# Kernel optimization log

Hardware: AMD Instinct MI355X
Metric: run time of the kernel (lower is better)

## Reference

```python
import jax, jax.numpy as jnp
import numpy as np

N, E, G = 50000, 800000, 512
HD, ED, GD, HID = 128, 64, 64, 128  # h_dim, e_dim, g_dim, hid_dim


def _mlp2(x, W1, b1, W2, b2, last_act):
    # Linear -> ReLU -> Linear (-> optional last activation)
    y = jax.nn.relu(x @ W1 + b1) @ W2 + b2
    return last_act(y) if last_act is not None else y


def setup_inputs() -> dict:
    key = jax.random.key(0)
    ks = list(jax.random.split(key, 24))
    ki = iter(ks)

    def p(shape):
        return (jax.random.normal(next(ki), shape, jnp.float32) * 0.02)

    inp = {
        "h": jax.random.normal(next(ki), (N, HD), jnp.float32),
        "e_index": jax.random.randint(next(ki), (2, E), 0, N),
        "e": jax.random.normal(next(ki), (E, ED), jnp.float32),
        "g": jax.random.normal(next(ki), (G, GD), jnp.float32),
        "batch": jnp.sort(jax.random.randint(next(ki), (N,), 0, G)),
        # fc_m: [2*HD+ED+GD, HID, HID], last_activation=relu
        "W_m1": p((2 * HD + ED + GD, HID)), "b_m1": jnp.zeros((HID,), jnp.float32),
        "W_m2": p((HID, HID)), "b_m2": jnp.zeros((HID,), jnp.float32),
        # fc_m_att: [HID, 1], sigmoid
        "W_ma": p((HID, 1)), "b_ma": jnp.zeros((1,), jnp.float32),
        # fc_e: [HID, ED, ED]
        "W_e1": p((HID, ED)), "b_e1": jnp.zeros((ED,), jnp.float32),
        "W_e2": p((ED, ED)), "b_e2": jnp.zeros((ED,), jnp.float32),
        # fc_h: [HD+HID+GD, HD, HD]
        "W_h1": p((HD + HID + GD, HD)), "b_h1": jnp.zeros((HD,), jnp.float32),
        "W_h2": p((HD, HD)), "b_h2": jnp.zeros((HD,), jnp.float32),
        # fc_h_att: [HD, 1]
        "W_ha": p((HD, 1)), "b_ha": jnp.zeros((1,), jnp.float32),
        # fc_g: [GD+HD, GD, GD]
        "W_g1": p((GD + HD, GD)), "b_g1": jnp.zeros((GD,), jnp.float32),
        "W_g2": p((GD, GD)), "b_g2": jnp.zeros((GD,), jnp.float32),
    }
    return inp


def reference(h, e_index, e, g, batch,
              W_m1, b_m1, W_m2, b_m2, W_ma, b_ma,
              W_e1, b_e1, W_e2, b_e2,
              W_h1, b_h1, W_h2, b_h2, W_ha, b_ha,
              W_g1, b_g1, W_g2, b_g2):
    src, dst = e_index[0], e_index[1]
    e_batch = batch[dst]

    # edge message: concat gathered endpoints + edge feat + gathered global
    m_cat = jnp.concatenate([h[src], h[dst], e, g[e_batch]], axis=1)  # [E, 2HD+ED+GD]
    m = jax.nn.relu(jax.nn.relu(m_cat @ W_m1 + b_m1) @ W_m2 + b_m2)   # [E, HID]
    m_att = jax.nn.sigmoid(m @ W_ma + b_ma)                            # [E, 1]

    e_update = _mlp2(m, W_e1, b_e1, W_e2, b_e2, None)                  # [E, ED]
    e_out = jax.nn.relu(e + e_update)

    m_aggr = jax.ops.segment_sum(m_att * m, dst, num_segments=h.shape[0])  # [N, HID]

    h_cat = jnp.concatenate([h, m_aggr, g[batch]], axis=1)             # [N, HD+HID+GD]
    h_update = _mlp2(h_cat, W_h1, b_h1, W_h2, b_h2, None)
    h_out = jax.nn.relu(h + h_update)                                  # [N, HD]
    h_att = h_out @ W_ha + b_ha                                        # [N, 1]

    h_aggr = jax.ops.segment_sum(h_att * h_out, batch, num_segments=g.shape[0])  # [G, HD]

    g_cat = jnp.concatenate([g, h_aggr], axis=1)                       # [G, GD+HD]
    g_update = _mlp2(g_cat, W_g1, b_g1, W_g2, b_g2, None)
    g_out = jax.nn.relu(g + g_update)

    return (h_out, e_out, g_out)
```

## Files before the change

### kernel.cpp

```cpp
#include <hip/hip_runtime.h>
#include <hip/hip_bf16.h>

#define NN 50000
#define NE 800000
#define NG 512
#define HD 128
#define ED 64
#define GD 64
#define HID 128

typedef __attribute__((ext_vector_type(8))) short short8;
typedef __attribute__((ext_vector_type(4))) float f32x4;

__device__ __forceinline__ short f2bf(float f) {
  union { float f; unsigned u; } v; v.f = f;
  unsigned r = v.u + 0x7fffu + ((v.u >> 16) & 1u);
  return (short)(r >> 16);
}

__device__ __forceinline__ short8 load_a8(const float* p) {
  const f32x4* q = (const f32x4*)p;
  f32x4 x0 = q[0], x1 = q[1];
  short8 r;
  r[0]=f2bf(x0[0]); r[1]=f2bf(x0[1]); r[2]=f2bf(x0[2]); r[3]=f2bf(x0[3]);
  r[4]=f2bf(x1[0]); r[5]=f2bf(x1[1]); r[6]=f2bf(x1[2]); r[7]=f2bf(x1[3]);
  return r;
}

__device__ __forceinline__ int swz(int row, int col, int rowBytes) {
  int b = row * rowBytes + col * 2;
  b ^= (row & 7) << 4;
  return b >> 1;
}

__global__ void pack_kernel(const float* __restrict__ Wm1, const float* __restrict__ Wm2,
                            const float* __restrict__ We1, const float* __restrict__ We2,
                            const float* __restrict__ Wh1, const float* __restrict__ Wh2,
                            short* __restrict__ out) {
  int gid = blockIdx.x * 256 + threadIdx.x;
  if (gid >= 135168) return;
  const float* W; int Ncol, base, idx;
  if (gid < 49152)       { W = Wm1; Ncol = 128; base = 0;      idx = gid; }
  else if (gid < 65536)  { W = Wm2; Ncol = 128; base = 49152;  idx = gid - 49152; }
  else if (gid < 73728)  { W = We1; Ncol = 64;  base = 65536;  idx = gid - 65536; }
  else if (gid < 77824)  { W = We2; Ncol = 64;  base = 73728;  idx = gid - 73728; }
  else if (gid < 118784) { W = Wh1; Ncol = 128; base = 77824;  idx = gid - 77824; }
  else                   { W = Wh2; Ncol = 128; base = 118784; idx = gid - 118784; }
  int k = idx / Ncol, n = idx % Ncol;
  out[base + (k >> 3) * Ncol * 8 + n * 8 + (k & 7)] = f2bf(W[idx]);
}

__global__ __launch_bounds__(256) void edge_kernel(
    const float* __restrict__ h, const int* __restrict__ ei,
    const float* __restrict__ e, const float* __restrict__ g,
    const int* __restrict__ batch,
    const short* __restrict__ pWm1, const float* __restrict__ bm1,
    const short* __restrict__ pWm2, const float* __restrict__ bm2,
    const float* __restrict__ Wma, const float* __restrict__ bma,
    const short* __restrict__ pWe1, const float* __restrict__ be1,
    const short* __restrict__ pWe2, const float* __restrict__ be2,
    float* __restrict__ e_out, float* __restrict__ m_aggr) {
  __shared__ short lds_m[4][16 * 128];
  __shared__ short lds_t[4][16 * 64];

  const int wave = threadIdx.x >> 6;
  const int lane = threadIdx.x & 63;
  const int row16 = lane & 15;
  const int quad = lane >> 4;
  const int ebase = blockIdx.x * 64 + wave * 16;

  const int eidA = ebase + row16;
  const int srcA = ei[eidA];
  const int dstA = ei[NE + eidA];
  const int gbA = batch[dstA];

  const float* seg0 = h + (size_t)srcA * HD;
  const float* seg1 = h + (size_t)dstA * HD;
  const float* seg2 = e + (size_t)eidA * ED;
  const float* seg3 = g + (size_t)gbA * GD;

  f32x4 acc[8];
#pragma unroll
  for (int t = 0; t < 8; ++t) acc[t] = (f32x4)0.0f;
#pragma unroll
  for (int c = 0; c < 12; ++c) {
    const float* src; int off;
    if (c < 4)       { src = seg0; off = c * 32; }
    else if (c < 8)  { src = seg1; off = (c - 4) * 32; }
    else if (c < 10) { src = seg2; off = (c - 8) * 32; }
    else             { src = seg3; off = (c - 10) * 32; }
    short8 a = load_a8(src + off + quad * 8);
    const short* bp = pWm1 + (size_t)(c * 4 + quad) * HID * 8 + row16 * 8;
#pragma unroll
    for (int t = 0; t < 8; ++t) {
      short8 b = *(const short8*)(bp + t * 16 * 8);
      acc[t] = __builtin_amdgcn_mfma_f32_16x16x32_bf16(a, b, acc[t], 0, 0, 0);
    }
  }
#pragma unroll
  for (int t = 0; t < 8; ++t) {
    float b1 = bm1[t * 16 + row16];
#pragma unroll
    for (int r = 0; r < 4; ++r) {
      float y = fmaxf(acc[t][r] + b1, 0.f);
      lds_m[wave][swz(quad * 4 + r, t * 16 + row16, 256)] = f2bf(y);
    }
  }
  __syncthreads();

  f32x4 acc2[8];
#pragma unroll
  for (int t = 0; t < 8; ++t) acc2[t] = (f32x4)0.0f;
#pragma unroll
  for (int c = 0; c < 4; ++c) {
    short8 a = *(const short8*)&lds_m[wave][swz(row16, c * 32 + quad * 8, 256)];
    const short* bp = pWm2 + 49152 * 0 + (size_t)(c * 4 + quad) * HID * 8 + row16 * 8;
#pragma unroll
    for (int t = 0; t < 8; ++t) {
      short8 b = *(const short8*)(bp + t * 16 * 8);
      acc2[t] = __builtin_amdgcn_mfma_f32_16x16x32_bf16(a, b, acc2[t], 0, 0, 0);
    }
  }
  __syncthreads();
  float mval[8][4];
#pragma unroll
  for (int t = 0; t < 8; ++t) {
    float b2 = bm2[t * 16 + row16];
#pragma unroll
    for (int r = 0; r < 4; ++r) {
      float y = fmaxf(acc2[t][r] + b2, 0.f);
      mval[t][r] = y;
      lds_m[wave][swz(quad * 4 + r, t * 16 + row16, 256)] = f2bf(y);
    }
  }
  __syncthreads();

  float part[4] = {0.f, 0.f, 0.f, 0.f};
#pragma unroll
  for (int t = 0; t < 8; ++t) {
    float w = Wma[t * 16 + row16];
#pragma unroll
    for (int r = 0; r < 4; ++r) part[r] += mval[t][r] * w;
  }
#pragma unroll
  for (int s = 1; s < 16; s <<= 1) {
#pragma unroll
    for (int r = 0; r < 4; ++r) part[r] += __shfl_xor(part[r], s, 64);
  }
  float bma0 = bma[0];
  float attv[4];
#pragma unroll
  for (int r = 0; r < 4; ++r) attv[r] = 1.f / (1.f + __expf(-(part[r] + bma0)));

  int dstS[4];
#pragma unroll
  for (int r = 0; r < 4; ++r) dstS[r] = ei[NE + ebase + quad * 4 + r];
#pragma unroll
  for (int t = 0; t < 8; ++t)
#pragma unroll
    for (int r = 0; r < 4; ++r)
      atomicAdd(&m_aggr[(size_t)dstS[r] * HID + t * 16 + row16], attv[r] * mval[t][r]);

  f32x4 acc3[4];
#pragma unroll
  for (int t = 0; t < 4; ++t) acc3[t] = (f32x4)0.0f;
#pragma unroll
  for (int c = 0; c < 4; ++c) {
    short8 a = *(const short8*)&lds_m[wave][swz(row16, c * 32 + quad * 8, 256)];
    const short* bp = pWe1 + (size_t)(c * 4 + quad) * ED * 8 + row16 * 8;
#pragma unroll
    for (int t = 0; t < 4; ++t) {
      short8 b = *(const short8*)(bp + t * 16 * 8);
      acc3[t] = __builtin_amdgcn_mfma_f32_16x16x32_bf16(a, b, acc3[t], 0, 0, 0);
    }
  }
#pragma unroll
  for (int t = 0; t < 4; ++t) {
    float b1 = be1[t * 16 + row16];
#pragma unroll
    for (int r = 0; r < 4; ++r) {
      float y = fmaxf(acc3[t][r] + b1, 0.f);
      lds_t[wave][swz(quad * 4 + r, t * 16 + row16, 128)] = f2bf(y);
    }
  }
  __syncthreads();

  f32x4 acc4[4];
#pragma unroll
  for (int t = 0; t < 4; ++t) acc4[t] = (f32x4)0.0f;
#pragma unroll
  for (int c = 0; c < 2; ++c) {
    short8 a = *(const short8*)&lds_t[wave][swz(row16, c * 32 + quad * 8, 128)];
    const short* bp = pWe2 + (size_t)(c * 4 + quad) * ED * 8 + row16 * 8;
#pragma unroll
    for (int t = 0; t < 4; ++t) {
      short8 b = *(const short8*)(bp + t * 16 * 8);
      acc4[t] = __builtin_amdgcn_mfma_f32_16x16x32_bf16(a, b, acc4[t], 0, 0, 0);
    }
  }
#pragma unroll
  for (int t = 0; t < 4; ++t) {
    float b2 = be2[t * 16 + row16];
#pragma unroll
    for (int r = 0; r < 4; ++r) {
      int erow = ebase + quad * 4 + r;
      int col = t * 16 + row16;
      float v = e[(size_t)erow * ED + col] + acc4[t][r] + b2;
      e_out[(size_t)erow * ED + col] = fmaxf(v, 0.f);
    }
  }
}

__global__ __launch_bounds__(256) void node_kernel(
    const float* __restrict__ h, const float* __restrict__ m_aggr,
    const float* __restrict__ g, const int* __restrict__ batch,
    const short* __restrict__ pWh1, const float* __restrict__ bh1,
    const short* __restrict__ pWh2, const float* __restrict__ bh2,
    const float* __restrict__ Wha, const float* __restrict__ bha,
    float* __restrict__ h_out, float* __restrict__ h_aggr) {
  __shared__ short lds_y[4][16 * 128];

  const int wave = threadIdx.x >> 6;
  const int lane = threadIdx.x & 63;
  const int row16 = lane & 15;
  const int quad = lane >> 4;
  const int nbase = blockIdx.x * 64 + wave * 16;

  int nA = nbase + row16;
  int nAc = nA < NN ? nA : NN - 1;
  int gbA = batch[nAc];
  const float* seg0 = h + (size_t)nAc * HD;
  const float* seg1 = m_aggr + (size_t)nAc * HID;
  const float* seg2 = g + (size_t)gbA * GD;

  f32x4 acc[8];
#pragma unroll
  for (int t = 0; t < 8; ++t) acc[t] = (f32x4)0.0f;
#pragma unroll
  for (int c = 0; c < 10; ++c) {
    const float* src; int off;
    if (c < 4)      { src = seg0; off = c * 32; }
    else if (c < 8) { src = seg1; off = (c - 4) * 32; }
    else            { src = seg2; off = (c - 8) * 32; }
    short8 a = load_a8(src + off + quad * 8);
    const short* bp = pWh1 + (size_t)(c * 4 + quad) * HD * 8 + row16 * 8;
#pragma unroll
    for (int t = 0; t < 8; ++t) {
      short8 b = *(const short8*)(bp + t * 16 * 8);
      acc[t] = __builtin_amdgcn_mfma_f32_16x16x32_bf16(a, b, acc[t], 0, 0, 0);
    }
  }
#pragma unroll
  for (int t = 0; t < 8; ++t) {
    float b1 = bh1[t * 16 + row16];
#pragma unroll
    for (int r = 0; r < 4; ++r) {
      float y = fmaxf(acc[t][r] + b1, 0.f);
      lds_y[wave][swz(quad * 4 + r, t * 16 + row16, 256)] = f2bf(y);
    }
  }
  __syncthreads();

  f32x4 acc2[8];
#pragma unroll
  for (int t = 0; t < 8; ++t) acc2[t] = (f32x4)0.0f;
#pragma unroll
  for (int c = 0; c < 4; ++c) {
    short8 a = *(const short8*)&lds_y[wave][swz(row16, c * 32 + quad * 8, 256)];
    const short* bp = pWh2 + (size_t)(c * 4 + quad) * HD * 8 + row16 * 8;
#pragma unroll
    for (int t = 0; t < 8; ++t) {
      short8 b = *(const short8*)(bp + t * 16 * 8);
      acc2[t] = __builtin_amdgcn_mfma_f32_16x16x32_bf16(a, b, acc2[t], 0, 0, 0);
    }
  }

  float hval[8][4];
  int nS[4];
#pragma unroll
  for (int r = 0; r < 4; ++r) nS[r] = nbase + quad * 4 + r;
#pragma unroll
  for (int t = 0; t < 8; ++t) {
    float b2 = bh2[t * 16 + row16];
#pragma unroll
    for (int r = 0; r < 4; ++r) {
      float v = 0.f;
      if (nS[r] < NN) {
        v = h[(size_t)nS[r] * HD + t * 16 + row16] + acc2[t][r] + b2;
        v = fmaxf(v, 0.f);
        h_out[(size_t)nS[r] * HD + t * 16 + row16] = v;
      }
      hval[t][r] = v;
    }
  }

  float part[4] = {0.f, 0.f, 0.f, 0.f};
#pragma unroll
  for (int t = 0; t < 8; ++t) {
    float w = Wha[t * 16 + row16];
#pragma unroll
    for (int r = 0; r < 4; ++r) part[r] += hval[t][r] * w;
  }
#pragma unroll
  for (int s = 1; s < 16; s <<= 1) {
#pragma unroll
    for (int r = 0; r < 4; ++r) part[r] += __shfl_xor(part[r], s, 64);
  }
  float bha0 = bha[0];
  int bS[4];
#pragma unroll
  for (int r = 0; r < 4; ++r) bS[r] = (nS[r] < NN) ? batch[nS[r]] : 0;
#pragma unroll
  for (int t = 0; t < 8; ++t)
#pragma unroll
    for (int r = 0; r < 4; ++r)
      if (nS[r] < NN)
        atomicAdd(&h_aggr[(size_t)bS[r] * HD + t * 16 + row16],
                  (part[r] + bha0) * hval[t][r]);
}

__global__ void g_kernel(const float* __restrict__ g, const float* __restrict__ h_aggr,
                         const float* __restrict__ Wg1, const float* __restrict__ bg1,
                         const float* __restrict__ Wg2, const float* __restrict__ bg2,
                         float* __restrict__ g_out) {
  __shared__ float cat[192];
  __shared__ float y1[64];
  int r = blockIdx.x;
  int t = threadIdx.x;
  cat[t] = g[(size_t)r * GD + t];
  cat[64 + t] = h_aggr[(size_t)r * HD + t];
  cat[128 + t] = h_aggr[(size_t)r * HD + 64 + t];
  __syncthreads();
  float a = bg1[t];
  for (int k = 0; k < 192; ++k) a += cat[k] * Wg1[k * 64 + t];
  y1[t] = fmaxf(a, 0.f);
  __syncthreads();
  float b = bg2[t];
  for (int k = 0; k < 64; ++k) b += y1[k] * Wg2[k * 64 + t];
  float v = g[(size_t)r * GD + t] + b;
  g_out[(size_t)r * GD + t] = fmaxf(v, 0.f);
}

extern "C" void kernel_launch(void* const* d_in, const int* in_sizes, int n_in,
                              void* d_out, int out_size, void* d_ws, size_t ws_size,
                              hipStream_t stream) {
  const float* h = (const float*)d_in[0];
  const int* ei = (const int*)d_in[1];
  const float* e = (const float*)d_in[2];
  const float* g = (const float*)d_in[3];
  const int* batch = (const int*)d_in[4];
  const float* Wm1 = (const float*)d_in[5];
  const float* bm1 = (const float*)d_in[6];
  const float* Wm2 = (const float*)d_in[7];
  const float* bm2 = (const float*)d_in[8];
  const float* Wma = (const float*)d_in[9];
  const float* bma = (const float*)d_in[10];
  const float* We1 = (const float*)d_in[11];
  const float* be1 = (const float*)d_in[12];
  const float* We2 = (const float*)d_in[13];
  const float* be2 = (const float*)d_in[14];
  const float* Wh1 = (const float*)d_in[15];
  const float* bh1 = (const float*)d_in[16];
  const float* Wh2 = (const float*)d_in[17];
  const float* bh2 = (const float*)d_in[18];
  const float* Wha = (const float*)d_in[19];
  const float* bha = (const float*)d_in[20];
  const float* Wg1 = (const float*)d_in[21];
  const float* bg1 = (const float*)d_in[22];
  const float* Wg2 = (const float*)d_in[23];
  const float* bg2 = (const float*)d_in[24];

  float* out = (float*)d_out;
  float* h_out = out;
  float* e_out = out + (size_t)NN * HD;
  float* g_out = e_out + (size_t)NE * ED;

  char* ws = (char*)d_ws;
  float* m_aggr = (float*)ws;
  float* h_aggr = (float*)(ws + 25600000);
  short* packed = (short*)(ws + 25862144);
  short* pWm1 = packed;
  short* pWm2 = packed + 49152;
  short* pWe1 = packed + 65536;
  short* pWe2 = packed + 73728;
  short* pWh1 = packed + 77824;
  short* pWh2 = packed + 118784;

  hipMemsetAsync(m_aggr, 0, (size_t)NN * HID * 4, stream);
  hipMemsetAsync(h_aggr, 0, (size_t)NG * HD * 4, stream);

  pack_kernel<<<(135168 + 255) / 256, 256, 0, stream>>>(Wm1, Wm2, We1, We2, Wh1, Wh2, packed);

  edge_kernel<<<NE / 64, 256, 0, stream>>>(h, ei, e, g, batch,
                                           pWm1, bm1, pWm2, bm2, Wma, bma,
                                           pWe1, be1, pWe2, be2, e_out, m_aggr);

  node_kernel<<<(NN + 63) / 64, 256, 0, stream>>>(h, m_aggr, g, batch,
                                                  pWh1, bh1, pWh2, bh2, Wha, bha,
                                                  h_out, h_aggr);

  g_kernel<<<NG, 64, 0, stream>>>(g, h_aggr, Wg1, bg1, Wg2, bg2, g_out);
}
```

Baseline: 755.0 us.

## Sort edges by destination and replace per-element atomics with block segmented reduction

Adds a counting sort of edges by destination node (count, single-block scan, scatter) so that each edge block processes edges grouped by dst. Attention-weighted messages are staged in LDS as bf16 and reduced per destination segment by 128 threads. Only boundary segments use atomics; segments fully inside the block are written with plain stores. The same segmented reduction replaces the per-element atomics into h_aggr in the node kernel, and several block barriers around wave-private LDS are dropped. In exchange it adds preprocessing kernels, scattered e/e_out row access through the permutation, and bf16 rounding of the aggregated contributions.

```diff
diff --git a/kernel.cpp b/kernel.cpp
--- a/kernel.cpp
+++ b/kernel.cpp
@@ -16,6 +16,12 @@
   union { float f; unsigned u; } v; v.f = f;
   unsigned r = v.u + 0x7fffu + ((v.u >> 16) & 1u);
   return (short)(r >> 16);
+}
+
+__device__ __forceinline__ float bf2f(short s) {
+  union { unsigned u; float f; } v;
+  v.u = ((unsigned)(unsigned short)s) << 16;
+  return v.f;
 }
 
 __device__ __forceinline__ short8 load_a8(const float* p) {
@@ -50,10 +56,44 @@
   out[base + (k >> 3) * Ncol * 8 + n * 8 + (k & 7)] = f2bf(W[idx]);
 }
 
+__global__ void count_kernel(const int* __restrict__ ei, int* __restrict__ deg) {
+  int i = blockIdx.x * 256 + threadIdx.x;
+  if (i < NE) atomicAdd(&deg[ei[NE + i]], 1);
+}
+
+__global__ __launch_bounds__(1024) void scan_kernel(int* __restrict__ deg) {
+  __shared__ int psum[1024];
+  const int CH = 49;
+  int t = threadIdx.x;
+  int lo = t * CH, hi = lo + CH; if (hi > NN) hi = NN; if (lo > NN) lo = NN;
+  int s = 0;
+  for (int i = lo; i < hi; ++i) s += deg[i];
+  psum[t] = s;
+  __syncthreads();
+  for (int d = 1; d < 1024; d <<= 1) {
+    int v = (t >= d) ? psum[t - d] : 0;
+    __syncthreads();
+    psum[t] += v;
+    __syncthreads();
+  }
+  int run = (t == 0) ? 0 : psum[t - 1];
+  for (int i = lo; i < hi; ++i) { int v = deg[i]; deg[i] = run; run += v; }
+}
+
+__global__ void scatter_kernel(const int* __restrict__ ei, int* __restrict__ off,
+                               int* __restrict__ elist) {
+  int i = blockIdx.x * 256 + threadIdx.x;
+  if (i < NE) {
+    int d = ei[NE + i];
+    int p = atomicAdd(&off[d], 1);
+    elist[p] = i;
+  }
+}
+
 __global__ __launch_bounds__(256) void edge_kernel(
     const float* __restrict__ h, const int* __restrict__ ei,
     const float* __restrict__ e, const float* __restrict__ g,
-    const int* __restrict__ batch,
+    const int* __restrict__ batch, const int* __restrict__ elist,
     const short* __restrict__ pWm1, const float* __restrict__ bm1,
     const short* __restrict__ pWm2, const float* __restrict__ bm2,
     const float* __restrict__ Wma, const float* __restrict__ bma,
@@ -62,17 +102,20 @@
     float* __restrict__ e_out, float* __restrict__ m_aggr) {
   __shared__ short lds_m[4][16 * 128];
   __shared__ short lds_t[4][16 * 64];
+  __shared__ short lds_w[64 * 132];
+  __shared__ int sdst[64];
 
   const int wave = threadIdx.x >> 6;
   const int lane = threadIdx.x & 63;
   const int row16 = lane & 15;
   const int quad = lane >> 4;
-  const int ebase = blockIdx.x * 64 + wave * 16;
-
-  const int eidA = ebase + row16;
+  const int pbase = blockIdx.x * 64 + wave * 16;
+
+  const int eidA = elist[pbase + row16];
   const int srcA = ei[eidA];
   const int dstA = ei[NE + eidA];
   const int gbA = batch[dstA];
+  if (quad == 0) sdst[wave * 16 + row16] = dstA;
 
   const float* seg0 = h + (size_t)srcA * HD;
   const float* seg1 = h + (size_t)dstA * HD;
@@ -106,7 +149,6 @@
       lds_m[wave][swz(quad * 4 + r, t * 16 + row16, 256)] = f2bf(y);
     }
   }
-  __syncthreads();
 
   f32x4 acc2[8];
 #pragma unroll
@@ -114,14 +156,14 @@
 #pragma unroll
   for (int c = 0; c < 4; ++c) {
     short8 a = *(const short8*)&lds_m[wave][swz(row16, c * 32 + quad * 8, 256)];
-    const short* bp = pWm2 + 49152 * 0 + (size_t)(c * 4 + quad) * HID * 8 + row16 * 8;
+    const short* bp = pWm2 + (size_t)(c * 4 + quad) * HID * 8 + row16 * 8;
 #pragma unroll
     for (int t = 0; t < 8; ++t) {
       short8 b = *(const short8*)(bp + t * 16 * 8);
       acc2[t] = __builtin_amdgcn_mfma_f32_16x16x32_bf16(a, b, acc2[t], 0, 0, 0);
     }
   }
-  __syncthreads();
+
   float mval[8][4];
 #pragma unroll
   for (int t = 0; t < 8; ++t) {
@@ -133,7 +175,6 @@
       lds_m[wave][swz(quad * 4 + r, t * 16 + row16, 256)] = f2bf(y);
     }
   }
-  __syncthreads();
 
   float part[4] = {0.f, 0.f, 0.f, 0.f};
 #pragma unroll
@@ -152,14 +193,33 @@
 #pragma unroll
   for (int r = 0; r < 4; ++r) attv[r] = 1.f / (1.f + __expf(-(part[r] + bma0)));
 
-  int dstS[4];
-#pragma unroll
-  for (int r = 0; r < 4; ++r) dstS[r] = ei[NE + ebase + quad * 4 + r];
 #pragma unroll
   for (int t = 0; t < 8; ++t)
 #pragma unroll
     for (int r = 0; r < 4; ++r)
-      atomicAdd(&m_aggr[(size_t)dstS[r] * HID + t * 16 + row16], attv[r] * mval[t][r]);
+      lds_w[(wave * 16 + quad * 4 + r) * 132 + t * 16 + row16] = f2bf(attv[r] * mval[t][r]);
+
+  __syncthreads();
+
+  if (threadIdx.x < 128) {
+    int col = threadIdx.x;
+    int cur = sdst[0];
+    float sum = 0.f;
+    int segs = 0;
+#pragma unroll 1
+    for (int r = 0; r < 64; ++r) {
+      int d = sdst[r];
+      float v = bf2f(lds_w[r * 132 + col]);
+      if (d != cur) {
+        if (segs == 0) atomicAdd(&m_aggr[(size_t)cur * HID + col], sum);
+        else m_aggr[(size_t)cur * HID + col] = sum;
+        cur = d; sum = v; segs = r;
+      } else {
+        sum += v;
+      }
+    }
+    atomicAdd(&m_aggr[(size_t)cur * HID + col], sum);
+  }
 
   f32x4 acc3[4];
 #pragma unroll
@@ -183,7 +243,6 @@
       lds_t[wave][swz(quad * 4 + r, t * 16 + row16, 128)] = f2bf(y);
     }
   }
-  __syncthreads();
 
   f32x4 acc4[4];
 #pragma unroll
@@ -198,15 +257,17 @@
       acc4[t] = __builtin_amdgcn_mfma_f32_16x16x32_bf16(a, b, acc4[t], 0, 0, 0);
     }
   }
+  int eidS[4];
+#pragma unroll
+  for (int r = 0; r < 4; ++r) eidS[r] = elist[blockIdx.x * 64 + wave * 16 + quad * 4 + r];
 #pragma unroll
   for (int t = 0; t < 4; ++t) {
     float b2 = be2[t * 16 + row16];
 #pragma unroll
     for (int r = 0; r < 4; ++r) {
-      int erow = ebase + quad * 4 + r;
       int col = t * 16 + row16;
-      float v = e[(size_t)erow * ED + col] + acc4[t][r] + b2;
-      e_out[(size_t)erow * ED + col] = fmaxf(v, 0.f);
+      float v = e[(size_t)eidS[r] * ED + col] + acc4[t][r] + b2;
+      e_out[(size_t)eidS[r] * ED + col] = fmaxf(v, 0.f);
     }
   }
 }
@@ -219,6 +280,8 @@
     const float* __restrict__ Wha, const float* __restrict__ bha,
     float* __restrict__ h_out, float* __restrict__ h_aggr) {
   __shared__ short lds_y[4][16 * 128];
+  __shared__ short lds_w2[64 * 132];
+  __shared__ int sbat[64];
 
   const int wave = threadIdx.x >> 6;
   const int lane = threadIdx.x & 63;
@@ -229,6 +292,7 @@
   int nA = nbase + row16;
   int nAc = nA < NN ? nA : NN - 1;
   int gbA = batch[nAc];
+  if (quad == 0) sbat[wave * 16 + row16] = (nA < NN) ? gbA : -1;
   const float* seg0 = h + (size_t)nAc * HD;
   const float* seg1 = m_aggr + (size_t)nAc * HID;
   const float* seg2 = g + (size_t)gbA * GD;
@@ -259,7 +323,6 @@
       lds_y[wave][swz(quad * 4 + r, t * 16 + row16, 256)] = f2bf(y);
     }
   }
-  __syncthreads();
 
   f32x4 acc2[8];
 #pragma unroll
@@ -307,16 +370,36 @@
     for (int r = 0; r < 4; ++r) part[r] += __shfl_xor(part[r], s, 64);
   }
   float bha0 = bha[0];
-  int bS[4];
-#pragma unroll
-  for (int r = 0; r < 4; ++r) bS[r] = (nS[r] < NN) ? batch[nS[r]] : 0;
 #pragma unroll
   for (int t = 0; t < 8; ++t)
 #pragma unroll
     for (int r = 0; r < 4; ++r)
-      if (nS[r] < NN)
-        atomicAdd(&h_aggr[(size_t)bS[r] * HD + t * 16 + row16],
-                  (part[r] + bha0) * hval[t][r]);
+      lds_w2[(wave * 16 + quad * 4 + r) * 132 + t * 16 + row16] =
+          f2bf((part[r] + bha0) * hval[t][r]);
+
+  __syncthreads();
+
+  if (threadIdx.x < 128) {
+    int col = threadIdx.x;
+    int cur = sbat[0];
+    float sum = 0.f;
+    int segs = 0;
+#pragma unroll 1
+    for (int r = 0; r < 64; ++r) {
+      int d = sbat[r];
+      float v = bf2f(lds_w2[r * 132 + col]);
+      if (d != cur) {
+        if (cur >= 0) {
+          if (segs == 0) atomicAdd(&h_aggr[(size_t)cur * HD + col], sum);
+          else h_aggr[(size_t)cur * HD + col] = sum;
+        }
+        cur = d; sum = v; segs = r;
+      } else {
+        sum += v;
+      }
+    }
+    if (cur >= 0) atomicAdd(&h_aggr[(size_t)cur * HD + col], sum);
+  }
 }
 
 __global__ void g_kernel(const float* __restrict__ g, const float* __restrict__ h_aggr,
@@ -379,6 +462,8 @@
   float* m_aggr = (float*)ws;
   float* h_aggr = (float*)(ws + 25600000);
   short* packed = (short*)(ws + 25862144);
+  int* deg      = (int*)(ws + 26132480);
+  int* elist    = (int*)(ws + 26332480);
   short* pWm1 = packed;
   short* pWm2 = packed + 49152;
   short* pWe1 = packed + 65536;
@@ -388,10 +473,14 @@
 
   hipMemsetAsync(m_aggr, 0, (size_t)NN * HID * 4, stream);
   hipMemsetAsync(h_aggr, 0, (size_t)NG * HD * 4, stream);
+  hipMemsetAsync(deg, 0, (size_t)NN * 4, stream);
 
   pack_kernel<<<(135168 + 255) / 256, 256, 0, stream>>>(Wm1, Wm2, We1, We2, Wh1, Wh2, packed);
-
-  edge_kernel<<<NE / 64, 256, 0, stream>>>(h, ei, e, g, batch,
+  count_kernel<<<(NE + 255) / 256, 256, 0, stream>>>(ei, deg);
+  scan_kernel<<<1, 1024, 0, stream>>>(deg);
+  scatter_kernel<<<(NE + 255) / 256, 256, 0, stream>>>(ei, deg, elist);
+
+  edge_kernel<<<NE / 64, 256, 0, stream>>>(h, ei, e, g, batch, elist,
                                            pWm1, bm1, pWm2, bm2, Wma, bma,
                                            pWe1, be1, pWe2, be2, e_out, m_aggr);
 
```

Result: faster. 692.0 us (-8.3%).
